# Kernel tuning notes

Measured on AMD Instinct MI355X. Metric: run time of the kernel, lower is better.

The kernel has to match this reference:

```python
import jax, jax.numpy as jnp
import numpy as np

S, B, D, DV = 2048, 16, 128, 128


def setup_inputs() -> dict:
    key = jax.random.key(0)
    kq, kk, kv = jax.random.split(key, 3)
    return {
        "query": jax.random.normal(kq, (S, B, D), dtype=jnp.float32),
        "key": jax.random.normal(kk, (S, B, D), dtype=jnp.float32),
        "value": jax.random.normal(kv, (S, B, DV), dtype=jnp.float32),
    }


def reference(query, key, value):
    # sim: [B, S_q, S_k]
    d = key.shape[-1]
    sim = jnp.einsum('sbd,tbd->bst', query, key) / jnp.sqrt(jnp.asarray(d, query.dtype))
    # causal mask: disallow attending to future positions (strictly upper triangle)
    sq, sk = sim.shape[-2], sim.shape[-1]
    causal = jnp.tril(jnp.ones((sq, sk), dtype=bool))  # [S_q, S_k]
    sim = jnp.where(causal[None, :, :], sim, -jnp.inf)
    a = jax.nn.softmax(sim, axis=-1)  # dropout omitted (eval mode, p=0)
    # context: [S_q, B, D_v]
    context = jnp.einsum('bst,tbe->sbe', a, value)
    return context
```

## Files before the change

kernel.cpp:

```cpp
#include <hip/hip_runtime.h>
#include <stdint.h>

#define SS 2048
#define BB 16
#define DD 128
#define DVV 128
#define BQ 32
#define BK 32
#define NTILES (SS / BK)
#define TILE_HW 4096

typedef __attribute__((ext_vector_type(8))) short short8;
typedef __attribute__((ext_vector_type(4))) float float4v;

typedef __attribute__((address_space(1))) const void glob_cv;
typedef __attribute__((address_space(3))) void lds_v;

__device__ __forceinline__ short f2bf(float f) {
  union { float f; uint32_t u; } x;
  x.f = f;
  uint32_t r = x.u + 0x7fffu + ((x.u >> 16) & 1u);
  return (short)(r >> 16);
}
__device__ __forceinline__ float bf2f(short h) {
  union { uint32_t u; float f; } y;
  y.u = ((uint32_t)(uint16_t)h) << 16;
  return y.f;
}

__device__ __forceinline__ int kappa(int quad, int j) {
  return (j < 4) ? (quad * 4 + j) : (16 + quad * 4 + (j - 4));
}

__global__ __launch_bounds__(256) void conv_kv(
    const float* __restrict__ kg, const float* __restrict__ vg,
    short* __restrict__ kimg, short* __restrict__ vimg) {
  __shared__ short tile[BK][136];
  const int t = blockIdx.x, b = blockIdx.y;
  if (blockIdx.z == 0) {
    short* out = kimg + ((size_t)(b * NTILES + t)) * TILE_HW;
#pragma unroll
    for (int p = 0; p < 2; ++p) {
      const int ch = threadIdx.x + p * 256;
      const int key = ch >> 4, c = ch & 15;
      const float* src = kg + ((size_t)(t * BK + key) * BB + b) * DD + c * 8;
      float4v f0 = *(const float4v*)src;
      float4v f1 = *(const float4v*)(src + 4);
      short8 s;
#pragma unroll
      for (int i = 0; i < 4; ++i) { s[i] = f2bf(f0[i]); s[4 + i] = f2bf(f1[i]); }
      *(short8*)(out + key * 128 + ((c ^ (key & 7)) * 8)) = s;
    }
  } else {
    short* out = vimg + ((size_t)(b * NTILES + t)) * TILE_HW;
#pragma unroll
    for (int p = 0; p < 2; ++p) {
      const int ch = threadIdx.x + p * 256;
      const int key = ch >> 4, fc = ch & 15;
      const float* src = vg + ((size_t)(t * BK + key) * BB + b) * DVV + fc * 8;
      float4v f0 = *(const float4v*)src;
      float4v f1 = *(const float4v*)(src + 4);
      short8 s;
#pragma unroll
      for (int i = 0; i < 4; ++i) { s[i] = f2bf(f0[i]); s[4 + i] = f2bf(f1[i]); }
      *(short8*)&tile[key][fc * 8] = s;
    }
    __syncthreads();
#pragma unroll
    for (int p = 0; p < 2; ++p) {
      const int idx = threadIdx.x + p * 256;
      const int nt = idx >> 6, quad = (idx >> 4) & 3, mm = idx & 15;
      const int dv = nt * 16 + mm;
      short8 s;
#pragma unroll
      for (int j = 0; j < 8; ++j) s[j] = tile[kappa(quad, j)][dv];
      *(short8*)(out + idx * 8) = s;
    }
  }
}

__global__ __launch_bounds__(256) void attn_fwd(
    const float* __restrict__ qg, const short* __restrict__ kimg,
    const short* __restrict__ vimg, float* __restrict__ og) {
  __shared__ __align__(16) short smem[4 * TILE_HW];
  short* const sKb = smem;
  short* const sVb = smem + 2 * TILE_HW;

  const int tid   = threadIdx.x;
  const int wave  = tid >> 6;
  const int qwave = wave & 1;
  const int tpar  = wave >> 1;
  const int lane  = tid & 63;
  const int m     = lane & 15;
  const int quad  = lane >> 4;
  const int bid   = blockIdx.x;
  const int half = bid >> 9, idx = bid & 511;
  const int qt   = half ? (idx >> 4) : (63 - (idx >> 4));
  const int b    = idx & 15;
  const int qw   = qt * BQ + qwave * 16;
  const int qrow = qw + m;

  const float cscale = 0.08838834764831845f * 1.4426950408889634f;
  short8 qfrag[4];
#pragma unroll
  for (int ks = 0; ks < 4; ++ks) {
    const float* qp = qg + ((size_t)qrow * BB + b) * DD + ks * 32 + quad * 8;
    float4v f0 = *(const float4v*)qp;
    float4v f1 = *(const float4v*)(qp + 4);
    short8 f;
#pragma unroll
    for (int i = 0; i < 4; ++i) { f[i] = f2bf(f0[i] * cscale); f[4 + i] = f2bf(f1[i] * cscale); }
    qfrag[ks] = f;
  }

  float4v oacc[8];
#pragma unroll
  for (int i = 0; i < 8; ++i) oacc[i] = (float4v){0.f, 0.f, 0.f, 0.f};
  float psum = 0.f;

  const short* tsrc = (qwave ? vimg : kimg) + (size_t)b * NTILES * TILE_HW + lane * 8;
  short* const sdst = (qwave ? sVb : sKb) + tpar * TILE_HW;

  const int ntile  = qt + 1;
  const int nround = (ntile + 1) >> 1;

  for (int r = 0; r < nround; ++r) {
    const int t = 2 * r + tpar;
    __syncthreads();
    if (t < ntile) {
      const short* src = tsrc + (size_t)t * TILE_HW;
#pragma unroll
      for (int j = 0; j < 8; ++j)
        __builtin_amdgcn_global_load_lds((glob_cv*)(src + j * 512),
                                         (lds_v*)(sdst + j * 512), 16, 0, 0);
    }
    __syncthreads();

    if (t < ntile) {
      const short* kb = sKb + tpar * TILE_HW;
      const short* vb = sVb + tpar * TILE_HW;

      float4v s0 = {0.f, 0.f, 0.f, 0.f}, s1 = {0.f, 0.f, 0.f, 0.f};
#pragma unroll
      for (int ks = 0; ks < 4; ++ks) {
        const int c = ks * 4 + quad;
        short8 kf0 = *(const short8*)&kb[m * 128 + ((c ^ (m & 7)) * 8)];
        short8 kf1 = *(const short8*)&kb[(16 + m) * 128 + ((c ^ (m & 7)) * 8)];
        s0 = __builtin_amdgcn_mfma_f32_16x16x32_bf16(kf0, qfrag[ks], s0, 0, 0, 0);
        s1 = __builtin_amdgcn_mfma_f32_16x16x32_bf16(kf1, qfrag[ks], s1, 0, 0, 0);
      }
      float sv[8];
#pragma unroll
      for (int rr = 0; rr < 4; ++rr) { sv[rr] = s0[rr]; sv[4 + rr] = s1[rr]; }

      const int kt0 = t * BK;
      if (kt0 + BK - 1 > qw) {
#pragma unroll
        for (int j = 0; j < 8; ++j)
          if (kt0 + kappa(quad, j) > qrow) sv[j] = -1e30f;
      }

      short8 pfrag;
#pragma unroll
      for (int j = 0; j < 8; ++j) {
        float p = exp2f(sv[j]);
        short h = f2bf(p);
        pfrag[j] = h;
        psum += bf2f(h);
      }

#pragma unroll
      for (int nt = 0; nt < 8; ++nt) {
        short8 vf = *(const short8*)&vb[nt * 512 + lane * 8];
        oacc[nt] = __builtin_amdgcn_mfma_f32_16x16x32_bf16(pfrag, vf, oacc[nt], 0, 0, 0);
      }
    }
  }

  __syncthreads();
  float* const cw = (float*)smem;
  if (tpar == 1) {
    float* p = cw + (size_t)(qwave * 64 + lane) * 36;
#pragma unroll
    for (int nt = 0; nt < 8; ++nt) *(float4v*)(p + nt * 4) = oacc[nt];
    p[32] = psum;
  }
  __syncthreads();
  if (tpar == 0) {
    const float* p = cw + (size_t)(qwave * 64 + lane) * 36;
#pragma unroll
    for (int nt = 0; nt < 8; ++nt) oacc[nt] += *(const float4v*)(p + nt * 4);
    psum += p[32];

    float l = psum;
    l += __shfl_xor(l, 16, 64);
    l += __shfl_xor(l, 32, 64);
    const float linv = 1.0f / l;
    float l4[4];
#pragma unroll
    for (int rr = 0; rr < 4; ++rr) l4[rr] = __shfl(linv, quad * 4 + rr, 64);
#pragma unroll
    for (int rr = 0; rr < 4; ++rr) {
      const int qgl = qw + quad * 4 + rr;
      float* op = og + ((size_t)qgl * BB + b) * DVV + m;
#pragma unroll
      for (int nt = 0; nt < 8; ++nt) op[nt * 16] = oacc[nt][rr] * l4[rr];
    }
  }
}

extern "C" void kernel_launch(void* const* d_in, const int* in_sizes, int n_in,
                              void* d_out, int out_size, void* d_ws, size_t ws_size,
                              hipStream_t stream) {
  const float* q = (const float*)d_in[0];
  const float* k = (const float*)d_in[1];
  const float* v = (const float*)d_in[2];
  float* out = (float*)d_out;
  short* kimg = (short*)d_ws;
  short* vimg = kimg + (size_t)BB * NTILES * TILE_HW;

  conv_kv<<<dim3(NTILES, BB, 2), 256, 0, stream>>>(k, v, kimg, vimg);
  attn_fwd<<<dim3(SS / BQ * BB), 256, 0, stream>>>(q, kimg, vimg, out);
}
```

Before: 134.5 us.

## Load K/V fragments directly from global in MFMA order, dropping LDS staging

The preprocessing kernel now writes K as well as V into a per-lane fragment-ordered image, so the attention kernel can read its MFMA operands straight from global memory with coalesced 16-byte loads. This removes the per-tile LDS staging and the two block barriers per round, letting each wave pair run its key tiles independently. The change also sets a minimum-occupancy launch bound, remaps blocks into four phases that interleave long and short causal rows with a batch permutation, and uses a packed bf16 convert instruction for the probabilities. In exchange, K/V reuse across the two query waves now depends on L1/L2 caching instead of shared memory, and register pressure is constrained by the occupancy hint.

```diff
diff --git a/kernel.cpp b/kernel.cpp
--- a/kernel.cpp
+++ b/kernel.cpp
@@ -13,19 +13,11 @@
 typedef __attribute__((ext_vector_type(8))) short short8;
 typedef __attribute__((ext_vector_type(4))) float float4v;
 
-typedef __attribute__((address_space(1))) const void glob_cv;
-typedef __attribute__((address_space(3))) void lds_v;
-
 __device__ __forceinline__ short f2bf(float f) {
   union { float f; uint32_t u; } x;
   x.f = f;
   uint32_t r = x.u + 0x7fffu + ((x.u >> 16) & 1u);
   return (short)(r >> 16);
-}
-__device__ __forceinline__ float bf2f(short h) {
-  union { uint32_t u; float f; } y;
-  y.u = ((uint32_t)(uint16_t)h) << 16;
-  return y.f;
 }
 
 __device__ __forceinline__ int kappa(int quad, int j) {
@@ -37,54 +29,41 @@
     short* __restrict__ kimg, short* __restrict__ vimg) {
   __shared__ short tile[BK][136];
   const int t = blockIdx.x, b = blockIdx.y;
-  if (blockIdx.z == 0) {
-    short* out = kimg + ((size_t)(b * NTILES + t)) * TILE_HW;
+  const float* src_base = (blockIdx.z == 0) ? kg : vg;
+  short* out = ((blockIdx.z == 0) ? kimg : vimg) + ((size_t)(b * NTILES + t)) * TILE_HW;
 #pragma unroll
-    for (int p = 0; p < 2; ++p) {
-      const int ch = threadIdx.x + p * 256;
-      const int key = ch >> 4, c = ch & 15;
-      const float* src = kg + ((size_t)(t * BK + key) * BB + b) * DD + c * 8;
-      float4v f0 = *(const float4v*)src;
-      float4v f1 = *(const float4v*)(src + 4);
-      short8 s;
+  for (int p = 0; p < 2; ++p) {
+    const int ch = threadIdx.x + p * 256;
+    const int key = ch >> 4, c = ch & 15;
+    const float* src = src_base + ((size_t)(t * BK + key) * BB + b) * DD + c * 8;
+    float4v f0 = *(const float4v*)src;
+    float4v f1 = *(const float4v*)(src + 4);
+    short8 s;
 #pragma unroll
-      for (int i = 0; i < 4; ++i) { s[i] = f2bf(f0[i]); s[4 + i] = f2bf(f1[i]); }
-      *(short8*)(out + key * 128 + ((c ^ (key & 7)) * 8)) = s;
+    for (int i = 0; i < 4; ++i) { s[i] = f2bf(f0[i]); s[4 + i] = f2bf(f1[i]); }
+    *(short8*)&tile[key][c * 8] = s;
+  }
+  __syncthreads();
+#pragma unroll
+  for (int p = 0; p < 2; ++p) {
+    const int idx = threadIdx.x + p * 256;
+    const int j = idx >> 6, quad = (idx >> 4) & 3, mm = idx & 15;
+    short8 s;
+    if (blockIdx.z == 0) {
+      const int ks = j >> 1, half = j & 1;
+      s = *(const short8*)&tile[half * 16 + mm][(ks * 4 + quad) * 8];
+    } else {
+#pragma unroll
+      for (int jj = 0; jj < 8; ++jj) s[jj] = tile[kappa(quad, jj)][j * 16 + mm];
     }
-  } else {
-    short* out = vimg + ((size_t)(b * NTILES + t)) * TILE_HW;
-#pragma unroll
-    for (int p = 0; p < 2; ++p) {
-      const int ch = threadIdx.x + p * 256;
-      const int key = ch >> 4, fc = ch & 15;
-      const float* src = vg + ((size_t)(t * BK + key) * BB + b) * DVV + fc * 8;
-      float4v f0 = *(const float4v*)src;
-      float4v f1 = *(const float4v*)(src + 4);
-      short8 s;
-#pragma unroll
-      for (int i = 0; i < 4; ++i) { s[i] = f2bf(f0[i]); s[4 + i] = f2bf(f1[i]); }
-      *(short8*)&tile[key][fc * 8] = s;
-    }
-    __syncthreads();
-#pragma unroll
-    for (int p = 0; p < 2; ++p) {
-      const int idx = threadIdx.x + p * 256;
-      const int nt = idx >> 6, quad = (idx >> 4) & 3, mm = idx & 15;
-      const int dv = nt * 16 + mm;
-      short8 s;
-#pragma unroll
-      for (int j = 0; j < 8; ++j) s[j] = tile[kappa(quad, j)][dv];
-      *(short8*)(out + idx * 8) = s;
-    }
+    *(short8*)(out + idx * 8) = s;
   }
 }
 
-__global__ __launch_bounds__(256) void attn_fwd(
+__global__ __launch_bounds__(256, 4) void attn_fwd(
     const float* __restrict__ qg, const short* __restrict__ kimg,
     const short* __restrict__ vimg, float* __restrict__ og) {
-  __shared__ __align__(16) short smem[4 * TILE_HW];
-  short* const sKb = smem;
-  short* const sVb = smem + 2 * TILE_HW;
+  __shared__ __align__(16) float cw[128 * 36];
 
   const int tid   = threadIdx.x;
   const int wave  = tid >> 6;
@@ -94,10 +73,11 @@
   const int m     = lane & 15;
   const int quad  = lane >> 4;
   const int bid   = blockIdx.x;
-  const int half = bid >> 9, idx = bid & 511;
-  const int qt   = half ? (idx >> 4) : (63 - (idx >> 4));
-  const int b    = idx & 15;
-  const int qw   = qt * BQ + qwave * 16;
+  const int g  = (bid >> 4) & 15;
+  const int ph = bid >> 8;
+  const int b  = ((bid & 7) << 1) | ((bid >> 3) & 1);
+  const int qt = (ph == 0) ? 63 - g : (ph == 1) ? g : (ph == 2) ? 47 - g : 16 + g;
+  const int qw = qt * BQ + qwave * 16;
   const int qrow = qw + m;
 
   const float cscale = 0.08838834764831845f * 1.4426950408889634f;
@@ -118,67 +98,56 @@
   for (int i = 0; i < 8; ++i) oacc[i] = (float4v){0.f, 0.f, 0.f, 0.f};
   float psum = 0.f;
 
-  const short* tsrc = (qwave ? vimg : kimg) + (size_t)b * NTILES * TILE_HW + lane * 8;
-  short* const sdst = (qwave ? sVb : sKb) + tpar * TILE_HW;
+  const short* kt = kimg + (size_t)b * NTILES * TILE_HW + lane * 8;
+  const short* vt = vimg + (size_t)b * NTILES * TILE_HW + lane * 8;
+  const int ntile = qt + 1;
 
-  const int ntile  = qt + 1;
-  const int nround = (ntile + 1) >> 1;
+  for (int t = tpar; t < ntile; t += 2) {
+    const short* kp = kt + (size_t)t * TILE_HW;
+    const short* vp = vt + (size_t)t * TILE_HW;
 
-  for (int r = 0; r < nround; ++r) {
-    const int t = 2 * r + tpar;
-    __syncthreads();
-    if (t < ntile) {
-      const short* src = tsrc + (size_t)t * TILE_HW;
+    float4v s0 = {0.f, 0.f, 0.f, 0.f}, s1 = {0.f, 0.f, 0.f, 0.f};
+#pragma unroll
+    for (int ks = 0; ks < 4; ++ks) {
+      short8 kf0 = *(const short8*)(kp + (ks * 2 + 0) * 512);
+      short8 kf1 = *(const short8*)(kp + (ks * 2 + 1) * 512);
+      s0 = __builtin_amdgcn_mfma_f32_16x16x32_bf16(kf0, qfrag[ks], s0, 0, 0, 0);
+      s1 = __builtin_amdgcn_mfma_f32_16x16x32_bf16(kf1, qfrag[ks], s1, 0, 0, 0);
+    }
+    float sv[8];
+#pragma unroll
+    for (int rr = 0; rr < 4; ++rr) { sv[rr] = s0[rr]; sv[4 + rr] = s1[rr]; }
+
+    const int kt0 = t * BK;
+    if (kt0 + BK - 1 > qw) {
 #pragma unroll
       for (int j = 0; j < 8; ++j)
-        __builtin_amdgcn_global_load_lds((glob_cv*)(src + j * 512),
-                                         (lds_v*)(sdst + j * 512), 16, 0, 0);
+        if (kt0 + kappa(quad, j) > qrow) sv[j] = -1e30f;
     }
-    __syncthreads();
 
-    if (t < ntile) {
-      const short* kb = sKb + tpar * TILE_HW;
-      const short* vb = sVb + tpar * TILE_HW;
-
-      float4v s0 = {0.f, 0.f, 0.f, 0.f}, s1 = {0.f, 0.f, 0.f, 0.f};
+    union { short8 s8; uint32_t w[4]; } pf;
 #pragma unroll
-      for (int ks = 0; ks < 4; ++ks) {
-        const int c = ks * 4 + quad;
-        short8 kf0 = *(const short8*)&kb[m * 128 + ((c ^ (m & 7)) * 8)];
-        short8 kf1 = *(const short8*)&kb[(16 + m) * 128 + ((c ^ (m & 7)) * 8)];
-        s0 = __builtin_amdgcn_mfma_f32_16x16x32_bf16(kf0, qfrag[ks], s0, 0, 0, 0);
-        s1 = __builtin_amdgcn_mfma_f32_16x16x32_bf16(kf1, qfrag[ks], s1, 0, 0, 0);
-      }
-      float sv[8];
-#pragma unroll
-      for (int rr = 0; rr < 4; ++rr) { sv[rr] = s0[rr]; sv[4 + rr] = s1[rr]; }
-
-      const int kt0 = t * BK;
-      if (kt0 + BK - 1 > qw) {
-#pragma unroll
-        for (int j = 0; j < 8; ++j)
-          if (kt0 + kappa(quad, j) > qrow) sv[j] = -1e30f;
-      }
-
-      short8 pfrag;
-#pragma unroll
-      for (int j = 0; j < 8; ++j) {
-        float p = exp2f(sv[j]);
-        short h = f2bf(p);
-        pfrag[j] = h;
-        psum += bf2f(h);
-      }
+    for (int jp = 0; jp < 4; ++jp) {
+      float p0 = exp2f(sv[2 * jp]);
+      float p1 = exp2f(sv[2 * jp + 1]);
+      uint32_t w;
+      asm("v_cvt_pk_bf16_f32 %0, %1, %2" : "=v"(w) : "v"(p0), "v"(p1));
+      pf.w[jp] = w;
+      union { uint32_t u; float f; } lo, hi;
+      lo.u = w << 16;
+      hi.u = w & 0xffff0000u;
+      psum += lo.f;
+      psum += hi.f;
+    }
+    const short8 pfrag = pf.s8;
 
 #pragma unroll
-      for (int nt = 0; nt < 8; ++nt) {
-        short8 vf = *(const short8*)&vb[nt * 512 + lane * 8];
-        oacc[nt] = __builtin_amdgcn_mfma_f32_16x16x32_bf16(pfrag, vf, oacc[nt], 0, 0, 0);
-      }
+    for (int nt = 0; nt < 8; ++nt) {
+      short8 vf = *(const short8*)(vp + nt * 512);
+      oacc[nt] = __builtin_amdgcn_mfma_f32_16x16x32_bf16(pfrag, vf, oacc[nt], 0, 0, 0);
     }
   }
 
-  __syncthreads();
-  float* const cw = (float*)smem;
   if (tpar == 1) {
     float* p = cw + (size_t)(qwave * 64 + lane) * 36;
 #pragma unroll
```

New measurement: 144.4 us. +7.4%, slower.
